# Kernel optimization log

Measured on AMD Instinct MI355X. Metric: run time of the kernel, lower is better.

## Reference

```python
import jax, jax.numpy as jnp
import numpy as np

D, H, WIN, TEMP = 512, 8, 2, 1.0
DH = D // H
SCALE = DH ** -0.5
SHIFT = WIN // 2


def _ln(x, g, b):
    m = jnp.mean(x, -1, keepdims=True)
    v = jnp.mean(jnp.square(x - m), -1, keepdims=True)
    return (x - m) * jax.lax.rsqrt(v + 1e-5) * g + b


def _win_attn(q, k, v):
    a = jax.nn.softmax(jnp.einsum('nhqd,nhkd->nhqk', q * SCALE, k) / TEMP, axis=-1)
    return jnp.einsum('nhqk,nhkd->nhqd', a, v)


def _self_block(x, p):
    qkv_w, qkv_b, proj_w, proj_b, n1g, n1b, n2g, n2b = p
    b, t, d = x.shape
    sc = x
    xw = _ln(x, n1g, n1b).reshape(b * t // WIN, WIN, d)  # window partition
    qkv = (xw @ qkv_w + qkv_b).reshape(-1, WIN, 3, H, DH).transpose(2, 0, 3, 1, 4)
    o = _win_attn(qkv[0], qkv[1], qkv[2])
    o = o.transpose(0, 2, 1, 3).reshape(-1, WIN, d) @ proj_w + proj_b
    return _ln(o.reshape(b, t, d) + sc, n2g, n2b)  # window reverse + residual


def _self_tf(x, p):
    x = _self_block(x, p)
    x = jnp.roll(x, -SHIFT, axis=1)   # sequence_shift
    x = _self_block(x, p)
    return jnp.roll(x, SHIFT, axis=1)  # sequence_inverse_shift


def _cross_block(x, y, p):
    q_w, q_b, kv_w, kv_b, proj_w, proj_b, n1g, n1b, n2g, n2b = p
    b, t, d = x.shape
    sc = x
    xw = _ln(x, n1g, n1b).reshape(-1, WIN, d)
    yw = _ln(y, n1g, n1b).reshape(-1, WIN, d)  # shared pre_norm, as in source
    q = (xw @ q_w + q_b).reshape(-1, WIN, H, DH).transpose(0, 2, 1, 3)
    kv = (yw @ kv_w + kv_b).reshape(-1, WIN, 2, H, DH).transpose(2, 0, 3, 1, 4)
    o = _win_attn(q, kv[0], kv[1])
    o = o.transpose(0, 2, 1, 3).reshape(-1, WIN, d) @ proj_w + proj_b
    return _ln(o.reshape(b, t, d) + sc, n2g, n2b)


def _cross_tf(x, y, p):
    x = _cross_block(x, y, p)
    x = jnp.roll(x, -SHIFT, axis=1)
    x = _cross_block(x, jnp.roll(y, -SHIFT, axis=1), p)
    return jnp.roll(x, SHIFT, axis=1)


def setup_inputs() -> dict:
    key = jax.random.key(0)
    ks = iter(jax.random.split(key, 40))
    B, T = 16, 4096
    d = {
        'x': jax.random.normal(next(ks), (B, T, D), jnp.float32),
        'y': jax.random.normal(next(ks), (B, T, D), jnp.float32),
    }

    def w(shape):
        return jax.random.normal(next(ks), shape, jnp.float32) * 0.02

    for m in ('wa', 'wv'):  # within-modal audio / video
        d[m + '_qkv_w'] = w((D, 3 * D)); d[m + '_qkv_b'] = jnp.zeros((3 * D,), jnp.float32)
        d[m + '_proj_w'] = w((D, D));    d[m + '_proj_b'] = jnp.zeros((D,), jnp.float32)
        d[m + '_n1_g'] = jnp.ones((D,), jnp.float32); d[m + '_n1_b'] = jnp.zeros((D,), jnp.float32)
        d[m + '_n2_g'] = jnp.ones((D,), jnp.float32); d[m + '_n2_b'] = jnp.zeros((D,), jnp.float32)
    # shared cross-modal transformer
    d['cm_q_w'] = w((D, D));      d['cm_q_b'] = jnp.zeros((D,), jnp.float32)
    d['cm_kv_w'] = w((D, 2 * D)); d['cm_kv_b'] = jnp.zeros((2 * D,), jnp.float32)
    d['cm_proj_w'] = w((D, D));   d['cm_proj_b'] = jnp.zeros((D,), jnp.float32)
    d['cm_n1_g'] = jnp.ones((D,), jnp.float32); d['cm_n1_b'] = jnp.zeros((D,), jnp.float32)
    d['cm_n2_g'] = jnp.ones((D,), jnp.float32); d['cm_n2_b'] = jnp.zeros((D,), jnp.float32)
    return d


def reference(x, y,
              wa_qkv_w, wa_qkv_b, wa_proj_w, wa_proj_b, wa_n1_g, wa_n1_b, wa_n2_g, wa_n2_b,
              wv_qkv_w, wv_qkv_b, wv_proj_w, wv_proj_b, wv_n1_g, wv_n1_b, wv_n2_g, wv_n2_b,
              cm_q_w, cm_q_b, cm_kv_w, cm_kv_b, cm_proj_w, cm_proj_b, cm_n1_g, cm_n1_b, cm_n2_g, cm_n2_b):
    pa = (wa_qkv_w, wa_qkv_b, wa_proj_w, wa_proj_b, wa_n1_g, wa_n1_b, wa_n2_g, wa_n2_b)
    pv = (wv_qkv_w, wv_qkv_b, wv_proj_w, wv_proj_b, wv_n1_g, wv_n1_b, wv_n2_g, wv_n2_b)
    pc = (cm_q_w, cm_q_b, cm_kv_w, cm_kv_b, cm_proj_w, cm_proj_b, cm_n1_g, cm_n1_b, cm_n2_g, cm_n2_b)
    # args.s1_attn == 'all' path
    x = _self_tf(x, pa)
    y = _self_tf(y, pv)
    xc = _cross_tf(x, y, pc)
    yc = _cross_tf(y, x, pc)
    return jnp.stack([x + xc, y + yc])  # (2, B, T, D)
```

## Files before the change

### kernel.cpp

```cpp
#include <hip/hip_runtime.h>

typedef unsigned short u16;
typedef unsigned int u32;
typedef __attribute__((ext_vector_type(8))) short short8;
typedef __attribute__((ext_vector_type(4))) short short4v;
typedef __attribute__((ext_vector_type(4))) float f32x4;

#define D_MODEL 512
#define NH 8
#define TSEQ 4096
#define NB 16
#define NROWS (NB*TSEQ)
#define QK_SCALE 0.125f
#define KDIM 512
#define NKI (KDIM/32)

__device__ __forceinline__ float b2f(u16 u){
    union { float f; unsigned int i; } v; v.i = ((unsigned int)u) << 16; return v.f;
}
__device__ __forceinline__ u16 f2b(float f){
    union { float f; unsigned int i; } v; v.f = f;
    unsigned int r = v.i + 0x7FFFu + ((v.i >> 16) & 1u);
    return (u16)(r >> 16);
}

__device__ __forceinline__ void async_copy16(u16* lds, const u16* g){
    __builtin_amdgcn_global_load_lds(
        (const __attribute__((address_space(1))) u32*)g,
        (__attribute__((address_space(3))) u32*)lds, 16, 0, 0);
}

__global__ void wconv_kernel(const float* __restrict__ W, u16* __restrict__ Wt, int K, int N){
    int idx = blockIdx.x * 256 + threadIdx.x;
    if (idx >= K * N) return;
    int n = idx / K;
    int k = idx - n * K;
    Wt[idx] = f2b(W[(size_t)k * N + n]);
}

__global__ __launch_bounds__(256) void ln_kernel(
    const float* __restrict__ X, const float* __restrict__ g,
    const float* __restrict__ b, u16* __restrict__ out)
{
    int row  = blockIdx.x * 4 + (threadIdx.x >> 6);
    int lane = threadIdx.x & 63;
    size_t base = (size_t)row * D_MODEL + lane * 8;
    float4 x0 = *(const float4*)(X + base);
    float4 x1 = *(const float4*)(X + base + 4);
    float t[8] = {x0.x,x0.y,x0.z,x0.w,x1.x,x1.y,x1.z,x1.w};
    float s = 0.f, ss = 0.f;
    #pragma unroll
    for (int j = 0; j < 8; j++){ s += t[j]; ss += t[j]*t[j]; }
    #pragma unroll
    for (int m = 1; m < 64; m <<= 1){ s += __shfl_xor(s, m); ss += __shfl_xor(ss, m); }
    float mean = s * (1.f/D_MODEL);
    float var  = ss * (1.f/D_MODEL) - mean*mean;
    float rst  = rsqrtf(var + 1e-5f);
    float4 g0 = *(const float4*)(g + lane*8);
    float4 g1 = *(const float4*)(g + lane*8 + 4);
    float4 c0 = *(const float4*)(b + lane*8);
    float4 c1 = *(const float4*)(b + lane*8 + 4);
    float gv[8] = {g0.x,g0.y,g0.z,g0.w,g1.x,g1.y,g1.z,g1.w};
    float bv[8] = {c0.x,c0.y,c0.z,c0.w,c1.x,c1.y,c1.z,c1.w};
    short8 o;
    #pragma unroll
    for (int j = 0; j < 8; j++) o[j] = (short)f2b((t[j]-mean)*rst*gv[j] + bv[j]);
    *(short8*)(out + base) = o;
}

__global__ __launch_bounds__(256) void resln_kernel(
    const u16* __restrict__ P, const float* __restrict__ Xin,
    const float* __restrict__ Add,
    const float* __restrict__ g, const float* __restrict__ b,
    float* __restrict__ out,
    u16* __restrict__ lnout, const float* __restrict__ g2, const float* __restrict__ b2)
{
    int row  = blockIdx.x * 4 + (threadIdx.x >> 6);
    int lane = threadIdx.x & 63;
    size_t base = (size_t)row * D_MODEL + lane * 8;
    short8 pv = *(const short8*)(P + base);
    float4 x0 = *(const float4*)(Xin + base);
    float4 x1 = *(const float4*)(Xin + base + 4);
    float xr[8] = {x0.x,x0.y,x0.z,x0.w,x1.x,x1.y,x1.z,x1.w};
    float t[8];
    #pragma unroll
    for (int j = 0; j < 8; j++) t[j] = b2f((u16)pv[j]) + xr[j];
    float s = 0.f, ss = 0.f;
    #pragma unroll
    for (int j = 0; j < 8; j++){ s += t[j]; ss += t[j]*t[j]; }
    #pragma unroll
    for (int m = 1; m < 64; m <<= 1){ s += __shfl_xor(s, m); ss += __shfl_xor(ss, m); }
    float mean = s * (1.f/D_MODEL);
    float var  = ss * (1.f/D_MODEL) - mean*mean;
    float rst  = rsqrtf(var + 1e-5f);
    float4 g0 = *(const float4*)(g + lane*8);
    float4 g1 = *(const float4*)(g + lane*8 + 4);
    float4 c0 = *(const float4*)(b + lane*8);
    float4 c1 = *(const float4*)(b + lane*8 + 4);
    float gv[8] = {g0.x,g0.y,g0.z,g0.w,g1.x,g1.y,g1.z,g1.w};
    float bv[8] = {c0.x,c0.y,c0.z,c0.w,c1.x,c1.y,c1.z,c1.w};
    float o[8];
    #pragma unroll
    for (int j = 0; j < 8; j++) o[j] = (t[j]-mean)*rst*gv[j] + bv[j];

    if (lnout){
        float s2 = 0.f, ss2 = 0.f;
        #pragma unroll
        for (int j = 0; j < 8; j++){ s2 += o[j]; ss2 += o[j]*o[j]; }
        #pragma unroll
        for (int m = 1; m < 64; m <<= 1){ s2 += __shfl_xor(s2, m); ss2 += __shfl_xor(ss2, m); }
        float mean2 = s2 * (1.f/D_MODEL);
        float var2  = ss2 * (1.f/D_MODEL) - mean2*mean2;
        float rst2  = rsqrtf(var2 + 1e-5f);
        float4 g20 = *(const float4*)(g2 + lane*8);
        float4 g21 = *(const float4*)(g2 + lane*8 + 4);
        float4 b20 = *(const float4*)(b2 + lane*8);
        float4 b21 = *(const float4*)(b2 + lane*8 + 4);
        float g2v[8] = {g20.x,g20.y,g20.z,g20.w,g21.x,g21.y,g21.z,g21.w};
        float b2v[8] = {b20.x,b20.y,b20.z,b20.w,b21.x,b21.y,b21.z,b21.w};
        short8 lo;
        #pragma unroll
        for (int j = 0; j < 8; j++) lo[j] = (short)f2b((o[j]-mean2)*rst2*g2v[j] + b2v[j]);
        *(short8*)(lnout + base) = lo;
    }
    if (Add){
        float4 a0 = *(const float4*)(Add + base);
        float4 a1 = *(const float4*)(Add + base + 4);
        float av[8] = {a0.x,a0.y,a0.z,a0.w,a1.x,a1.y,a1.z,a1.w};
        #pragma unroll
        for (int j = 0; j < 8; j++) o[j] += av[j];
    }
    float4 r0 = {o[0],o[1],o[2],o[3]};
    float4 r1 = {o[4],o[5],o[6],o[7]};
    *(float4*)(out + base)     = r0;
    *(float4*)(out + base + 4) = r1;
}

__global__ __launch_bounds__(256) void qkvattn_kernel(
    const u16* __restrict__ A, const u16* __restrict__ Wt,
    const float* __restrict__ bias, u16* __restrict__ O, int shift)
{
    __shared__ __align__(16) u16 lds[2][20*512];
    int tid  = threadIdx.x;
    int lane = tid & 63;
    int wid  = tid >> 6;

    int bid  = blockIdx.x;
    int swz  = (bid & 7) * 512 + (bid >> 3);
    int head = swz >> 9;
    int rt   = swz & 511;
    int bt   = rt >> 5;
    int tb   = (rt & 31) * 128;

    f32x4 acc[2][12];
    f32x4 zero = {0.f,0.f,0.f,0.f};
    #pragma unroll
    for (int m = 0; m < 2; m++)
        #pragma unroll
        for (int n = 0; n < 12; n++) acc[m][n] = zero;

    int rr = lane >> 2, kc = (lane & 3) * 8;
    const u16* p[5];
    int cidb = wid * 5;
    #pragma unroll
    for (int q = 0; q < 5; q++){
        int cid = cidb + q;
        if (cid < 8){
            int i   = cid*16 + rr;
            int tok = (tb + shift + i) & (TSEQ-1);
            p[q] = A + ((size_t)bt * TSEQ + tok) * KDIM + kc;
        } else {
            int cb   = cid - 8;
            int wrow = (cb >> 2) * 512 + head*64 + (cb & 3)*16 + rr;
            p[q] = Wt + (size_t)wrow * KDIM + kc;
        }
    }

    int lrow = lane & 15;
    int lk   = (lane >> 4) * 8;
    int aoff = (wid*32 + lrow) * 32 + lk;
    int boff = 8*512 + lrow*32 + lk;

    #pragma unroll
    for (int q = 0; q < 5; q++){ async_copy16(&lds[0][(cidb+q)*512], p[q]); p[q] += 32; }
    asm volatile("s_waitcnt vmcnt(0)" ::: "memory");
    __syncthreads();

    #pragma unroll
    for (int t = 0; t < NKI; t++){
        const u16* cbuf = lds[t & 1];
        u16* nbuf = (u16*)lds[(t & 1) ^ 1];
        if (t < NKI-1){
            #pragma unroll
            for (int q = 0; q < 5; q++){ async_copy16(&nbuf[(cidb+q)*512], p[q]); p[q] += 32; }
        }
        short8 af[2], bf[12];
        #pragma unroll
        for (int m = 0; m < 2; m++) af[m] = *(const short8*)(cbuf + aoff + m*512);
        #pragma unroll
        for (int n = 0; n < 12; n++) bf[n] = *(const short8*)(cbuf + boff + n*512);
        #pragma unroll
        for (int m = 0; m < 2; m++)
            #pragma unroll
            for (int n = 0; n < 12; n++)
                acc[m][n] = __builtin_amdgcn_mfma_f32_16x16x32_bf16(af[m], bf[n], acc[m][n], 0, 0, 0);
        if (t < NKI-1){
            asm volatile("s_waitcnt vmcnt(0)" ::: "memory");
            __syncthreads();
        }
    }

    int g_ = lane >> 4, lc = lane & 15;
    float bq[4], bk[4], bv[4];
    #pragma unroll
    for (int n = 0; n < 4; n++){
        int d = head*64 + n*16 + lc;
        bq[n] = bias[d]; bk[n] = bias[512 + d]; bv[n] = bias[1024 + d];
    }
    #pragma unroll
    for (int m = 0; m < 2; m++){
        #pragma unroll
        for (int wnd = 0; wnd < 2; wnd++){
            int ja = 2*wnd, jb = ja + 1;
            float s00=0.f, s01=0.f, s10=0.f, s11=0.f;
            #pragma unroll
            for (int n = 0; n < 4; n++){
                float qa = acc[m][n][ja] + bq[n],  qb = acc[m][n][jb] + bq[n];
                float ka = acc[m][4+n][ja] + bk[n], kb = acc[m][4+n][jb] + bk[n];
                s00 += qa*ka; s01 += qa*kb; s10 += qb*ka; s11 += qb*kb;
            }
            #pragma unroll
            for (int msk = 1; msk < 16; msk <<= 1){
                s00 += __shfl_xor(s00, msk); s01 += __shfl_xor(s01, msk);
                s10 += __shfl_xor(s10, msk); s11 += __shfl_xor(s11, msk);
            }
            s00 *= QK_SCALE; s01 *= QK_SCALE; s10 *= QK_SCALE; s11 *= QK_SCALE;
            float m0 = fmaxf(s00, s01), m1 = fmaxf(s10, s11);
            float e00 = expf(s00-m0), e01 = expf(s01-m0);
            float e10 = expf(s10-m1), e11 = expf(s11-m1);
            float ia = 1.f/(e00+e01), ib = 1.f/(e10+e11);
            float a00 = e00*ia, a01 = e01*ia, a10 = e10*ib, a11 = e11*ib;
            int ra = wid*32 + m*16 + 4*g_ + ja;
            int ta = (tb + shift + ra) & (TSEQ-1);
            size_t growa = (size_t)bt * TSEQ + ta;
            size_t growb = (size_t)bt * TSEQ + ((ta + 1) & (TSEQ-1));
            #pragma unroll
            for (int n = 0; n < 4; n++){
                float va = acc[m][8+n][ja] + bv[n], vb = acc[m][8+n][jb] + bv[n];
                int col = head*64 + n*16 + lc;
                O[growa * D_MODEL + col] = f2b(a00*va + a01*vb);
                O[growb * D_MODEL + col] = f2b(a10*va + a11*vb);
            }
        }
    }
}

__global__ __launch_bounds__(512) void gemm256_kernel(
    const u16* __restrict__ A, const u16* __restrict__ Wt,
    const float* __restrict__ bias, u16* __restrict__ C, int N, int nN)
{
    __shared__ __align__(16) u16 sh[65536];
    int tid  = threadIdx.x;
    int lane = tid & 63;
    int wid  = tid >> 6;
    int wm   = wid >> 2, wn = wid & 3;

    int cpx = (int)gridDim.x >> 3;
    int swz = ((int)blockIdx.x & 7) * cpx + ((int)blockIdx.x >> 3);
    int row0 = (swz / nN) * 256;
    int col0 = (swz % nN) * 256;

    f32x4 acc[8][4];
    f32x4 zero = {0.f,0.f,0.f,0.f};
    #pragma unroll
    for (int m = 0; m < 8; m++)
        #pragma unroll
        for (int n = 0; n < 4; n++) acc[m][n] = zero;

    int lrow = lane & 15, khi = lane >> 4;
    int addrA[8], addrB[4];
    #pragma unroll
    for (int m = 0; m < 8; m++){
        int r = wm*128 + m*16 + lrow;
        addrA[m] = r*32 + ((khi ^ ((r>>1)&3)) << 3);
    }
    #pragma unroll
    for (int n = 0; n < 4; n++){
        int r = wn*64 + n*16 + lrow;
        addrB[n] = r*32 + ((khi ^ ((r>>1)&3)) << 3);
    }

    const u16* Ab = A  + (size_t)row0 * KDIM;
    const u16* Bb = Wt + (size_t)col0 * KDIM;
    int sr0 = (wid << 4) + (lane >> 2);
    int ss  = lane & 3;
    int sx  = (ss ^ ((sr0 >> 1) & 3)) << 3;

    #define STAGE_A(buf, t, kh) { \
        u16* d_ = &sh[(buf)*16384 + (kh)*8192 + wid*512]; \
        const u16* s_ = Ab + (size_t)sr0*KDIM + (t)*64 + (kh)*32 + sx; \
        async_copy16(d_, s_); \
        async_copy16(d_ + 4096, s_ + (size_t)128*KDIM); }
    #define STAGE_B(buf, t, kh) { \
        u16* d_ = &sh[32768 + (buf)*16384 + (kh)*8192 + wid*512]; \
        const u16* s_ = Bb + (size_t)sr0*KDIM + (t)*64 + (kh)*32 + sx; \
        async_copy16(d_, s_); \
        async_copy16(d_ + 4096, s_ + (size_t)128*KDIM); }

    #define COMPUTE(buf, kh) { \
        const u16* ca_ = &sh[(buf)*16384 + (kh)*8192]; \
        const u16* cb_ = ca_ + 32768; \
        short8 af[8], bf[4]; \
        _Pragma("unroll") \
        for (int m = 0; m < 8; m++) af[m] = *(const short8*)(ca_ + addrA[m]); \
        _Pragma("unroll") \
        for (int n = 0; n < 4; n++) bf[n] = *(const short8*)(cb_ + addrB[n]); \
        __builtin_amdgcn_s_setprio(1); \
        _Pragma("unroll") \
        for (int m = 0; m < 8; m++) \
            _Pragma("unroll") \
            for (int n = 0; n < 4; n++) \
                acc[m][n] = __builtin_amdgcn_mfma_f32_16x16x32_bf16(af[m], bf[n], acc[m][n], 0, 0, 0); \
        __builtin_amdgcn_s_setprio(0); }

    STAGE_A(0, 0, 0); STAGE_B(0, 0, 0);
    STAGE_A(0, 0, 1); STAGE_B(0, 0, 1);

    #pragma unroll
    for (int t = 0; t < 8; t++){
        int buf = t & 1;
        if (t < 7){
            STAGE_A(buf^1, t+1, 0); STAGE_B(buf^1, t+1, 0);
            STAGE_A(buf^1, t+1, 1); STAGE_B(buf^1, t+1, 1);
            asm volatile("s_waitcnt vmcnt(8)" ::: "memory");
        } else {
            asm volatile("s_waitcnt vmcnt(0)" ::: "memory");
        }
        __builtin_amdgcn_s_barrier();
        COMPUTE(buf, 0);
        COMPUTE(buf, 1);
        __builtin_amdgcn_s_barrier();
    }

    int g_ = lane >> 4, lc = lane & 15;
    #pragma unroll
    for (int n = 0; n < 4; n++){
        int c = col0 + wn*64 + n*16 + lc;
        float bvv = bias[c];
        #pragma unroll
        for (int m = 0; m < 8; m++){
            int r = row0 + wm*128 + m*16 + 4*g_;
            f32x4 v = acc[m][n];
            C[(size_t)(r+0) * N + c] = f2b(v[0] + bvv);
            C[(size_t)(r+1) * N + c] = f2b(v[1] + bvv);
            C[(size_t)(r+2) * N + c] = f2b(v[2] + bvv);
            C[(size_t)(r+3) * N + c] = f2b(v[3] + bvv);
        }
    }
    #undef STAGE_A
    #undef STAGE_B
    #undef COMPUTE
}

__global__ __launch_bounds__(256) void attn_cross_kernel(
    const u16* __restrict__ Q, const u16* __restrict__ KV,
    u16* __restrict__ O, int shift)
{
    int tsk  = blockIdx.x * 4 + (threadIdx.x >> 6);
    int lane = threadIdx.x & 63;
    int w  = tsk >> 1;
    int hb = tsk & 1;
    int bt = w >> 11;
    int wt = w & 2047;
    int t0 = (2*wt + shift) & (TSEQ - 1);
    int t1 = (t0 + 1) & (TSEQ - 1);
    size_t g0 = (size_t)bt * TSEQ + t0;
    size_t g1 = (size_t)bt * TSEQ + t1;
    int col = hb*256 + lane*4;
    short4v q0 = *(const short4v*)(Q  + g0*512  + col);
    short4v q1 = *(const short4v*)(Q  + g1*512  + col);
    short4v k0 = *(const short4v*)(KV + g0*1024 + col);
    short4v k1 = *(const short4v*)(KV + g1*1024 + col);
    short4v v0 = *(const short4v*)(KV + g0*1024 + 512 + col);
    short4v v1 = *(const short4v*)(KV + g1*1024 + 512 + col);
    float s00=0.f, s01=0.f, s10=0.f, s11=0.f;
    float v0f[4], v1f[4];
    #pragma unroll
    for (int j = 0; j < 4; j++){
        float qa = b2f((u16)q0[j]), qb = b2f((u16)q1[j]);
        float ka = b2f((u16)k0[j]), kb = b2f((u16)k1[j]);
        v0f[j] = b2f((u16)v0[j]); v1f[j] = b2f((u16)v1[j]);
        s00 += qa*ka; s01 += qa*kb; s10 += qb*ka; s11 += qb*kb;
    }
    #pragma unroll
    for (int m = 1; m < 16; m <<= 1){
        s00 += __shfl_xor(s00, m); s01 += __shfl_xor(s01, m);
        s10 += __shfl_xor(s10, m); s11 += __shfl_xor(s11, m);
    }
    s00 *= QK_SCALE; s01 *= QK_SCALE; s10 *= QK_SCALE; s11 *= QK_SCALE;
    float m0 = fmaxf(s00, s01), m1 = fmaxf(s10, s11);
    float e00 = expf(s00 - m0), e01 = expf(s01 - m0);
    float e10 = expf(s10 - m1), e11 = expf(s11 - m1);
    float ia = 1.f/(e00 + e01), ib = 1.f/(e10 + e11);
    float a00 = e00*ia, a01 = e01*ia, a10 = e10*ib, a11 = e11*ib;
    short4v o0, o1;
    #pragma unroll
    for (int j = 0; j < 4; j++){
        o0[j] = (short)f2b(a00*v0f[j] + a01*v1f[j]);
        o1[j] = (short)f2b(a10*v0f[j] + a11*v1f[j]);
    }
    *(short4v*)(O + g0*512 + col) = o0;
    *(short4v*)(O + g1*512 + col) = o1;
}

extern "C" void kernel_launch(void* const* d_in, const int* in_sizes, int n_in,
                              void* d_out, int out_size, void* d_ws, size_t ws_size,
                              hipStream_t stream)
{
    const float* x = (const float*)d_in[0];
    const float* y = (const float*)d_in[1];
    const float* wa_qkv_w = (const float*)d_in[2];  const float* wa_qkv_b = (const float*)d_in[3];
    const float* wa_proj_w= (const float*)d_in[4];  const float* wa_proj_b= (const float*)d_in[5];
    const float* wa_n1g   = (const float*)d_in[6];  const float* wa_n1b   = (const float*)d_in[7];
    const float* wa_n2g   = (const float*)d_in[8];  const float* wa_n2b   = (const float*)d_in[9];
    const float* wv_qkv_w = (const float*)d_in[10]; const float* wv_qkv_b = (const float*)d_in[11];
    const float* wv_proj_w= (const float*)d_in[12]; const float* wv_proj_b= (const float*)d_in[13];
    const float* wv_n1g   = (const float*)d_in[14]; const float* wv_n1b   = (const float*)d_in[15];
    const float* wv_n2g   = (const float*)d_in[16]; const float* wv_n2b   = (const float*)d_in[17];
    const float* cm_q_w   = (const float*)d_in[18]; const float* cm_q_b   = (const float*)d_in[19];
    const float* cm_kv_w  = (const float*)d_in[20]; const float* cm_kv_b  = (const float*)d_in[21];
    const float* cm_proj_w= (const float*)d_in[22]; const float* cm_proj_b= (const float*)d_in[23];
    const float* cm_n1g   = (const float*)d_in[24]; const float* cm_n1b   = (const float*)d_in[25];
    const float* cm_n2g   = (const float*)d_in[26]; const float* cm_n2b   = (const float*)d_in[27];

    char* ws = (char*)d_ws;
    const size_t SZ_F32 = (size_t)NROWS * D_MODEL * 4;
    const size_t SZ_B16 = (size_t)NROWS * D_MODEL * 2;
    float* F1  = (float*)(ws);
    float* XF  = (float*)(ws + SZ_F32);
    float* YF  = (float*)(ws + 2*SZ_F32);
    u16*   XN  = (u16*)  (ws + 3*SZ_F32);
    u16*   CN  = (u16*)  (ws + 3*SZ_F32 + SZ_B16);
    u16*   XLN = (u16*)  (ws + 3*SZ_F32 + 2*SZ_B16);
    u16*   YLN = (u16*)  (ws + 3*SZ_F32 + 3*SZ_B16);
    u16*   O   = (u16*)  (ws + 3*SZ_F32 + 4*SZ_B16);
    u16*   KVb = (u16*)  (ws + 3*SZ_F32 + 5*SZ_B16);
    u16*   WB  = (u16*)  (ws + 3*SZ_F32 + 8*SZ_B16);

    u16* PB = KVb;

    u16* wa_qkv_t  = WB;
    u16* wa_proj_t = wa_qkv_t  + 1536*512;
    u16* wv_qkv_t  = wa_proj_t + 512*512;
    u16* wv_proj_t = wv_qkv_t  + 1536*512;
    u16* cm_q_t    = wv_proj_t + 512*512;
    u16* cm_kv_t   = cm_q_t    + 512*512;
    u16* cm_proj_t = cm_kv_t   + 1024*512;

    auto conv = [&](const float* W, u16* Wt, int K, int N){
        int total = K * N;
        wconv_kernel<<<(total + 255) / 256, 256, 0, stream>>>(W, Wt, K, N);
    };
    conv(wa_qkv_w,  wa_qkv_t,  512, 1536);
    conv(wa_proj_w, wa_proj_t, 512, 512);
    conv(wv_qkv_w,  wv_qkv_t,  512, 1536);
    conv(wv_proj_w, wv_proj_t, 512, 512);
    conv(cm_q_w,    cm_q_t,    512, 512);
    conv(cm_kv_w,   cm_kv_t,   512, 1024);
    conv(cm_proj_w, cm_proj_t, 512, 512);

    const int lnGrid   = NROWS / 4;
    const int attnGrid = NROWS / 2 * 2 / 4;
    const int qaGrid   = (NROWS / 128) * NH;

    auto gemm = [&](const u16* Ain, const u16* Wt, const float* bias, u16* Cout, int N){
        int nN = N / 256;
        gemm256_kernel<<<(NROWS/256) * nN, 512, 0, stream>>>(Ain, Wt, bias, Cout, N, nN);
    };

    auto self_chain = [&](const float* in, float* outF, u16* outLN,
                          const u16* qkvT, const float* qkv_b,
                          const u16* projT, const float* proj_b,
                          const float* n1g, const float* n1b,
                          const float* n2g, const float* n2b){
        ln_kernel<<<lnGrid, 256, 0, stream>>>(in, n1g, n1b, XN);
        qkvattn_kernel<<<qaGrid, 256, 0, stream>>>(XN, qkvT, qkv_b, O, 0);
        gemm(O, projT, proj_b, PB, 512);
        resln_kernel<<<lnGrid, 256, 0, stream>>>(PB, in, nullptr, n2g, n2b, F1, XN, n1g, n1b);
        qkvattn_kernel<<<qaGrid, 256, 0, stream>>>(XN, qkvT, qkv_b, O, 1);
        gemm(O, projT, proj_b, PB, 512);
        resln_kernel<<<lnGrid, 256, 0, stream>>>(PB, F1, nullptr, n2g, n2b, outF, outLN, cm_n1g, cm_n1b);
    };

    self_chain(x, XF, XLN, wa_qkv_t, wa_qkv_b, wa_proj_t, wa_proj_b, wa_n1g, wa_n1b, wa_n2g, wa_n2b);
    self_chain(y, YF, YLN, wv_qkv_t, wv_qkv_b, wv_proj_t, wv_proj_b, wv_n1g, wv_n1b, wv_n2g, wv_n2b);

    float* out0 = (float*)d_out;
    float* out1 = out0 + (size_t)NROWS * D_MODEL;

    auto cross_chain = [&](const u16* qLN, const u16* kvLN, const float* resF, float* outF){
        gemm(kvLN, cm_kv_t, cm_kv_b, KVb, 1024);
        gemm(qLN,  cm_q_t,  cm_q_b,  XN,  512);
        attn_cross_kernel<<<attnGrid, 256, 0, stream>>>(XN, KVb, O, 0);
        gemm(O, cm_proj_t, cm_proj_b, XN, 512);
        resln_kernel<<<lnGrid, 256, 0, stream>>>(XN, resF, nullptr, cm_n2g, cm_n2b, F1, CN, cm_n1g, cm_n1b);
        gemm(CN, cm_q_t, cm_q_b, XN, 512);
        attn_cross_kernel<<<attnGrid, 256, 0, stream>>>(XN, KVb, O, 1);
        gemm(O, cm_proj_t, cm_proj_b, XN, 512);
        resln_kernel<<<lnGrid, 256, 0, stream>>>(XN, F1, resF, cm_n2g, cm_n2b, outF, nullptr, nullptr, nullptr);
    };

    cross_chain(XLN, YLN, XF, out0);
    cross_chain(YLN, XLN, YF, out1);
}
```

Measured before the change: 2.495 ms.

## Restructure GEMM mainloop into eight-phase interleaved load/compute schedule

Rewrites the 256x256 GEMM main loop into a finer-grained schedule. Each K-step of 64 is split into quadrant MFMA phases, and async global-to-LDS copies of individual 128-row half-tiles are interleaved between them, with barriers around each phase. The LDS layout becomes 128x64 half-tiles with a new XOR swizzle, and launch bounds now request two blocks per CU. The goal is better overlap of memory traffic with MFMA work and higher occupancy. The cost is many more barriers, and the requested occupancy may force register pressure or spills given the 128-float accumulator.

```diff
diff --git a/kernel.cpp b/kernel.cpp
--- a/kernel.cpp
+++ b/kernel.cpp
@@ -255,20 +255,21 @@
     }
 }
 
-__global__ __launch_bounds__(512) void gemm256_kernel(
+#define AOFc(buf,h) (((buf)*2+(h))*8192)
+#define BOFc(buf,h) (32768 + ((buf)*2+(h))*8192)
+
+__global__ __launch_bounds__(512, 2) void gemm256_kernel(
     const u16* __restrict__ A, const u16* __restrict__ Wt,
     const float* __restrict__ bias, u16* __restrict__ C, int N, int nN)
 {
     __shared__ __align__(16) u16 sh[65536];
-    int tid  = threadIdx.x;
-    int lane = tid & 63;
-    int wid  = tid >> 6;
-    int wm   = wid >> 2, wn = wid & 3;
-
-    int cpx = (int)gridDim.x >> 3;
-    int swz = ((int)blockIdx.x & 7) * cpx + ((int)blockIdx.x >> 3);
-    int row0 = (swz / nN) * 256;
-    int col0 = (swz % nN) * 256;
+    u16* sh_ = (u16*)sh;
+    const int tid = threadIdx.x, lane = tid & 63, wid = tid >> 6;
+    const int wm = wid >> 2, wn = wid & 3;
+    const int cpx = (int)gridDim.x >> 3;
+    const int swz = ((int)blockIdx.x & 7) * cpx + ((int)blockIdx.x >> 3);
+    const int row0 = (swz / nN) * 256;
+    const int col0 = (swz % nN) * 256;
 
     f32x4 acc[8][4];
     f32x4 zero = {0.f,0.f,0.f,0.f};
@@ -277,69 +278,94 @@
         #pragma unroll
         for (int n = 0; n < 4; n++) acc[m][n] = zero;
 
-    int lrow = lane & 15, khi = lane >> 4;
-    int addrA[8], addrB[4];
-    #pragma unroll
-    for (int m = 0; m < 8; m++){
-        int r = wm*128 + m*16 + lrow;
-        addrA[m] = r*32 + ((khi ^ ((r>>1)&3)) << 3);
-    }
-    #pragma unroll
-    for (int n = 0; n < 4; n++){
-        int r = wn*64 + n*16 + lrow;
-        addrB[n] = r*32 + ((khi ^ ((r>>1)&3)) << 3);
-    }
-
-    const u16* Ab = A  + (size_t)row0 * KDIM;
-    const u16* Bb = Wt + (size_t)col0 * KDIM;
-    int sr0 = (wid << 4) + (lane >> 2);
-    int ss  = lane & 3;
-    int sx  = (ss ^ ((sr0 >> 1) & 3)) << 3;
-
-    #define STAGE_A(buf, t, kh) { \
-        u16* d_ = &sh[(buf)*16384 + (kh)*8192 + wid*512]; \
-        const u16* s_ = Ab + (size_t)sr0*KDIM + (t)*64 + (kh)*32 + sx; \
-        async_copy16(d_, s_); \
-        async_copy16(d_ + 4096, s_ + (size_t)128*KDIM); }
-    #define STAGE_B(buf, t, kh) { \
-        u16* d_ = &sh[32768 + (buf)*16384 + (kh)*8192 + wid*512]; \
-        const u16* s_ = Bb + (size_t)sr0*KDIM + (t)*64 + (kh)*32 + sx; \
-        async_copy16(d_, s_); \
-        async_copy16(d_ + 4096, s_ + (size_t)128*KDIM); }
-
-    #define COMPUTE(buf, kh) { \
-        const u16* ca_ = &sh[(buf)*16384 + (kh)*8192]; \
-        const u16* cb_ = ca_ + 32768; \
-        short8 af[8], bf[4]; \
+    const int lrow = lane & 15, khi = lane >> 4;
+    const int swx   = (lrow & 4) << 2;
+    const int kcol0 = (khi*8) ^ swx;
+    const int kcol1 = (32 + khi*8) ^ swx;
+    const int aR0 = AOFc(0, wm) , aR1 = AOFc(1, wm);
+    const int bh  = wn >> 1;
+    const int bR0 = BOFc(0, bh), bR1 = BOFc(1, bh);
+    const int abase = lrow*64;
+    const int bbase = (wn & 1)*4096 + lrow*64;
+
+    const u16* Ag = A  + (size_t)row0 * KDIM;
+    const u16* Bg = Wt + (size_t)col0 * KDIM;
+    const int csrc = ((lane & 7) * 8) ^ (((lane >> 3) & 4) << 2);
+    const int srow = wid*16 + (lane >> 3);
+
+    short8 af[4][2], bf[4][2];
+
+    #define STG(dstOff, gp) { \
+        const u16* s1_ = (gp) + (size_t)srow*KDIM + csrc; \
+        u16* d1_ = sh_ + (dstOff) + wid*1024; \
+        async_copy16(d1_, s1_); \
+        async_copy16(d1_ + 512, s1_ + (size_t)8*KDIM); }
+    #define RDA(bufR, h) { \
+        const u16* p_ = sh_ + (bufR) + abase; \
         _Pragma("unroll") \
-        for (int m = 0; m < 8; m++) af[m] = *(const short8*)(ca_ + addrA[m]); \
+        for (int i_ = 0; i_ < 4; i_++){ \
+            af[i_][0] = *(const short8*)(p_ + ((h)*4+i_)*1024 + kcol0); \
+            af[i_][1] = *(const short8*)(p_ + ((h)*4+i_)*1024 + kcol1); } }
+    #define RDB(bufR, nh) { \
+        const u16* p_ = sh_ + (bufR) + bbase; \
         _Pragma("unroll") \
-        for (int n = 0; n < 4; n++) bf[n] = *(const short8*)(cb_ + addrB[n]); \
+        for (int j_ = 0; j_ < 2; j_++){ \
+            bf[(nh)*2+j_][0] = *(const short8*)(p_ + ((nh)*2+j_)*1024 + kcol0); \
+            bf[(nh)*2+j_][1] = *(const short8*)(p_ + ((nh)*2+j_)*1024 + kcol1); } }
+    #define MM(mh, nh) { \
         __builtin_amdgcn_s_setprio(1); \
         _Pragma("unroll") \
-        for (int m = 0; m < 8; m++) \
+        for (int m_ = 0; m_ < 4; m_++) \
             _Pragma("unroll") \
-            for (int n = 0; n < 4; n++) \
-                acc[m][n] = __builtin_amdgcn_mfma_f32_16x16x32_bf16(af[m], bf[n], acc[m][n], 0, 0, 0); \
+            for (int n_ = 0; n_ < 2; n_++){ \
+                acc[(mh)*4+m_][(nh)*2+n_] = __builtin_amdgcn_mfma_f32_16x16x32_bf16(af[m_][0], bf[(nh)*2+n_][0], acc[(mh)*4+m_][(nh)*2+n_], 0,0,0); \
+                acc[(mh)*4+m_][(nh)*2+n_] = __builtin_amdgcn_mfma_f32_16x16x32_bf16(af[m_][1], bf[(nh)*2+n_][1], acc[(mh)*4+m_][(nh)*2+n_], 0,0,0); } \
         __builtin_amdgcn_s_setprio(0); }
-
-    STAGE_A(0, 0, 0); STAGE_B(0, 0, 0);
-    STAGE_A(0, 0, 1); STAGE_B(0, 0, 1);
-
-    #pragma unroll
-    for (int t = 0; t < 8; t++){
-        int buf = t & 1;
-        if (t < 7){
-            STAGE_A(buf^1, t+1, 0); STAGE_B(buf^1, t+1, 0);
-            STAGE_A(buf^1, t+1, 1); STAGE_B(buf^1, t+1, 1);
-            asm volatile("s_waitcnt vmcnt(8)" ::: "memory");
-        } else {
-            asm volatile("s_waitcnt vmcnt(0)" ::: "memory");
-        }
-        __builtin_amdgcn_s_barrier();
-        COMPUTE(buf, 0);
-        COMPUTE(buf, 1);
-        __builtin_amdgcn_s_barrier();
+    #define BAR() { asm volatile("" ::: "memory"); __builtin_amdgcn_s_barrier(); asm volatile("" ::: "memory"); }
+    #define VMW4() asm volatile("s_waitcnt vmcnt(4)" ::: "memory")
+    #define VMW0() asm volatile("s_waitcnt vmcnt(0)" ::: "memory")
+
+    STG(BOFc(0,0), Bg);
+    STG(BOFc(0,1), Bg + (size_t)128*KDIM);
+    STG(AOFc(0,0), Ag);
+    STG(AOFc(0,1), Ag + (size_t)128*KDIM);
+    STG(BOFc(1,0), Bg + 64);
+    STG(BOFc(1,1), Bg + (size_t)128*KDIM + 64);
+    VMW4();
+    BAR();
+
+    #pragma unroll
+    for (int i = 0; i < 4; i++){
+        RDA(aR0, 0); RDB(bR0, 0);
+        STG(AOFc(1,0), Ag + (2*i+1)*64);
+        BAR(); MM(0,0); BAR();
+
+        RDB(bR0, 1);
+        STG(AOFc(1,1), Ag + (size_t)128*KDIM + (2*i+1)*64);
+        BAR(); MM(0,1); BAR();
+
+        RDA(aR0, 1);
+        if (i < 3) STG(BOFc(0,0), Bg + (2*i+2)*64);
+        BAR(); MM(1,0); BAR();
+
+        if (i < 3){ STG(BOFc(0,1), Bg + (size_t)128*KDIM + (2*i+2)*64); VMW4(); }
+        else      { VMW0(); }
+        BAR(); MM(1,1); BAR();
+
+        RDA(aR1, 0); RDB(bR1, 0);
+        if (i < 3) STG(AOFc(0,0), Ag + (2*i+2)*64);
+        BAR(); MM(0,0); BAR();
+
+        RDB(bR1, 1);
+        if (i < 3) STG(AOFc(0,1), Ag + (size_t)128*KDIM + (2*i+2)*64);
+        BAR(); MM(0,1); BAR();
+
+        RDA(aR1, 1);
+        if (i < 3) STG(BOFc(1,0), Bg + (2*i+3)*64);
+        BAR(); MM(1,0); BAR();
+
+        if (i < 3){ STG(BOFc(1,1), Bg + (size_t)128*KDIM + (2*i+3)*64); VMW4(); }
+        BAR(); MM(1,1); BAR();
     }
 
     int g_ = lane >> 4, lc = lane & 15;
@@ -357,9 +383,13 @@
             C[(size_t)(r+3) * N + c] = f2b(v[3] + bvv);
         }
     }
-    #undef STAGE_A
-    #undef STAGE_B
-    #undef COMPUTE
+    #undef STG
+    #undef RDA
+    #undef RDB
+    #undef MM
+    #undef BAR
+    #undef VMW4
+    #undef VMW0
 }
 
 __global__ __launch_bounds__(256) void attn_cross_kernel(
```

New measurement: 2.357 ms. 5.6% less time.
